# Kernel tuning notes

Measured on AMD Instinct MI355X. Metric: run time of the kernel, lower is better.

## Reference

```python
import jax, jax.numpy as jnp
import numpy as np

N_NODES = 50000
N_EDGES = 1_600_000
D = 64


def setup_inputs() -> dict:
    key = jax.random.key(0)
    k1, k2, k3, k4 = jax.random.split(key, 4)
    x = jax.random.normal(k1, (N_NODES, D), dtype=jnp.float32)
    # Glorot-ish scale for the dense transform
    weight = jax.random.normal(k2, (D, D), dtype=jnp.float32) * (1.0 / np.sqrt(D))
    bias = jnp.zeros((D,), dtype=jnp.float32)
    src = jax.random.randint(k3, (N_EDGES,), 0, N_NODES, dtype=jnp.int32)
    dst = jax.random.randint(k4, (N_EDGES,), 0, N_NODES, dtype=jnp.int32)
    t = jnp.zeros((1,), dtype=jnp.float32)
    return {"t": t, "x": x, "weight": weight, "bias": bias, "src": src, "dst": dst}


def reference(t, x, weight, bias, src, dst):
    # GCDEFunc.forward(t, x) -> GCNLayer(x); dropout=0 (eval / ODE solve).
    n = x.shape[0]
    # symmetric GCN normalization: 1/sqrt(in_degree), 0 for isolated nodes
    deg = jax.ops.segment_sum(jnp.ones_like(dst, dtype=x.dtype), dst, num_segments=n)
    norm = jnp.where(deg > 0, jax.lax.rsqrt(jnp.maximum(deg, 1.0)), 0.0)[:, None]  # [N,1]
    h = x @ weight                 # [N,D] dense transform
    h = h * norm                   # src-side normalization
    # SpMM: sum messages copy_src(h) over incoming edges
    h = jax.ops.segment_sum(h[src], dst, num_segments=n)  # [N,D]
    h = h * norm + bias            # dst-side normalization + bias
    return jax.nn.softplus(h)      # smooth activation for ODE dynamics
```

## Files before the change

### kernel.cpp

```cpp
#include <hip/hip_runtime.h>
#include <hip/hip_fp16.h>

constexpr int N = 50000;
constexpr int D = 64;
constexpr int E = 1600000;
constexpr int NBUCK = (N + 127) / 128;
constexpr int CAP = 4608;
constexpr int BTHREADS = 512;
constexpr int BBLOCKS = 512;
constexpr int EPB = E / BBLOCKS;
constexpr int CPT = (EPB + BTHREADS - 1) / BTHREADS;

__global__ void k_init(int* __restrict__ cursor) {
    int t = threadIdx.x;
    if (t < NBUCK) cursor[t] = t * CAP;
}

__global__ void k_bucket(const int* __restrict__ src, const int* __restrict__ dst,
                         int* __restrict__ cursor, unsigned* __restrict__ packed) {
    __shared__ int lh[NBUCK];
    __shared__ int scanI[NBUCK];
    __shared__ int wsum[8];
    __shared__ int lb[NBUCK];
    __shared__ unsigned stage[EPB];
    int tid = threadIdx.x;
    if (tid < NBUCK) lh[tid] = 0;
    __syncthreads();
    int base_e = blockIdx.x * EPB;
    unsigned pk[CPT];
    int bn[CPT], rk[CPT];
#pragma unroll
    for (int i = 0; i < CPT; ++i) {
        int idx = i * BTHREADS + tid;
        if (idx < EPB) {
            int e = base_e + idx;
            int d = dst[e];
            int s = src[e];
            bn[i] = d >> 7;
            pk[i] = ((unsigned)d << 16) | (unsigned)s;
            rk[i] = atomicAdd(&lh[bn[i]], 1);
        } else bn[i] = -1;
    }
    __syncthreads();
    int w = tid >> 6, l = tid & 63;
    int v = (tid < NBUCK) ? lh[tid] : 0;
    for (int off = 1; off < 64; off <<= 1) {
        int t = __shfl_up(v, off, 64);
        if (l >= off) v += t;
    }
    if (tid < NBUCK) scanI[tid] = v;
    if (l == 63) wsum[w] = v;
    __syncthreads();
    if (tid < 64) {
        int s = (tid < 8) ? wsum[tid] : 0;
        for (int off = 1; off < 8; off <<= 1) {
            int t = __shfl_up(s, off, 64);
            if (tid >= off) s += t;
        }
        if (tid < 8) wsum[tid] = s;
    }
    __syncthreads();
    if (tid < NBUCK && w > 0) scanI[tid] += wsum[w - 1];
    if (tid < NBUCK) {
        int c = lh[tid];
        lb[tid] = c ? atomicAdd(&cursor[tid], c) : 0;
    }
    __syncthreads();
#pragma unroll
    for (int i = 0; i < CPT; ++i) {
        if (bn[i] >= 0) {
            int eb = (bn[i] == 0) ? 0 : scanI[bn[i] - 1];
            stage[eb + rk[i]] = pk[i];
        }
    }
    __syncthreads();
    for (int j = tid; j < EPB; j += BTHREADS) {
        unsigned vv = stage[j];
        int bk = vv >> 23;
        int eb = (bk == 0) ? 0 : scanI[bk - 1];
        packed[lb[bk] + (j - eb)] = vv;
    }
}

__global__ void k_csr(const int* __restrict__ cursor, const unsigned* __restrict__ packed,
                      unsigned short* __restrict__ csr, int* __restrict__ rowptr,
                      int* __restrict__ rowend, float* __restrict__ norm) {
    __shared__ int cnt[128];
    __shared__ int sm[128];
    __shared__ int cur[128];
    __shared__ unsigned short stage[CAP];
    int b = blockIdx.x, tid = threadIdx.x;
    if (tid < 128) cnt[tid] = 0;
    __syncthreads();
    int beg = b * CAP;
    int m = cursor[b] - beg;
    for (int j = tid; j < m; j += 1024)
        atomicAdd(&cnt[(packed[beg + j] >> 16) & 127], 1);
    __syncthreads();
    if (tid < 64) {
        int a = cnt[2 * tid], c1 = cnt[2 * tid + 1];
        int s = a + c1;
        for (int off = 1; off < 64; off <<= 1) {
            int t = __shfl_up(s, off, 64);
            if (tid >= off) s += t;
        }
        sm[2 * tid + 1] = s;
        sm[2 * tid] = s - c1;
    }
    __syncthreads();
    if (tid < 128) {
        int incl = sm[tid];
        int excl = incl - cnt[tid];
        int node = b * 128 + tid;
        if (node < N) {
            rowptr[node] = beg + excl;
            rowend[node] = beg + incl;
            norm[node] = cnt[tid] ? rsqrtf((float)cnt[tid]) : 0.0f;
        }
        cur[tid] = excl;
    }
    __syncthreads();
    for (int j = tid; j < m; j += 1024) {
        unsigned p = packed[beg + j];
        int slot = atomicAdd(&cur[(p >> 16) & 127], 1);
        stage[slot] = (unsigned short)(p & 0xFFFFu);
    }
    __syncthreads();
    unsigned* du = (unsigned*)(csr + beg);
    const unsigned* su = (const unsigned*)stage;
    int mu = m >> 1;
    for (int k = tid; k < mu; k += 1024) du[k] = su[k];
    if ((m & 1) && tid == 0) csr[beg + m - 1] = stage[m - 1];
}

__global__ __launch_bounds__(256)
void k_gemm(const float* __restrict__ x, const float* __restrict__ W,
            const float* __restrict__ norm, __half* __restrict__ h2) {
    __shared__ float xT[64 * 68];
    __shared__ float Wl[64 * 64];
    int tid = threadIdx.x;
    int rowbase = blockIdx.x * 64;
    {
        const float4* W4 = (const float4*)W;
        float4* Wl4 = (float4*)Wl;
#pragma unroll
        for (int i = 0; i < 4; ++i)
            Wl4[i * 256 + tid] = W4[i * 256 + tid];
    }
    {
        int rr = tid >> 2;
        int c0 = (tid & 3) * 16;
        int row = rowbase + rr;
        if (row >= N) row = N - 1;
        const float4* xr = (const float4*)(x + (size_t)row * 64 + c0);
#pragma unroll
        for (int i = 0; i < 4; ++i) {
            float4 v = xr[i];
            int c = c0 + i * 4;
            xT[(c + 0) * 68 + rr] = v.x;
            xT[(c + 1) * 68 + rr] = v.y;
            xT[(c + 2) * 68 + rr] = v.z;
            xT[(c + 3) * 68 + rr] = v.w;
        }
    }
    __syncthreads();
    int tx = tid & 15;
    int ty = tid >> 4;
    float acc[4][4] = {};
#pragma unroll 8
    for (int k = 0; k < 64; ++k) {
        float4 xv = *(const float4*)&xT[k * 68 + ty * 4];
        float4 wv = *(const float4*)&Wl[k * 64 + tx * 4];
        acc[0][0] = fmaf(xv.x, wv.x, acc[0][0]);
        acc[0][1] = fmaf(xv.x, wv.y, acc[0][1]);
        acc[0][2] = fmaf(xv.x, wv.z, acc[0][2]);
        acc[0][3] = fmaf(xv.x, wv.w, acc[0][3]);
        acc[1][0] = fmaf(xv.y, wv.x, acc[1][0]);
        acc[1][1] = fmaf(xv.y, wv.y, acc[1][1]);
        acc[1][2] = fmaf(xv.y, wv.z, acc[1][2]);
        acc[1][3] = fmaf(xv.y, wv.w, acc[1][3]);
        acc[2][0] = fmaf(xv.z, wv.x, acc[2][0]);
        acc[2][1] = fmaf(xv.z, wv.y, acc[2][1]);
        acc[2][2] = fmaf(xv.z, wv.z, acc[2][2]);
        acc[2][3] = fmaf(xv.z, wv.w, acc[2][3]);
        acc[3][0] = fmaf(xv.w, wv.x, acc[3][0]);
        acc[3][1] = fmaf(xv.w, wv.y, acc[3][1]);
        acc[3][2] = fmaf(xv.w, wv.z, acc[3][2]);
        acc[3][3] = fmaf(xv.w, wv.w, acc[3][3]);
    }
#pragma unroll
    for (int i = 0; i < 4; ++i) {
        int row = rowbase + ty * 4 + i;
        if (row < N) {
            float nr = norm[row];
            __half2 p0 = __floats2half2_rn(acc[i][0] * nr, acc[i][1] * nr);
            __half2 p1 = __floats2half2_rn(acc[i][2] * nr, acc[i][3] * nr);
            __half2* dst2 = (__half2*)(h2 + (size_t)row * 64 + tx * 4);
            dst2[0] = p0;
            dst2[1] = p1;
        }
    }
}

__global__ void k_aggregate(const int* __restrict__ rowptr, const int* __restrict__ rowend,
                            const unsigned short* __restrict__ csr,
                            const __half* __restrict__ h2, const float* __restrict__ norm,
                            const float* __restrict__ bias, float* __restrict__ out) {
    int node = blockIdx.x * 4 + (threadIdx.x >> 6);
    int lane = threadIdx.x & 63;
    int half = lane >> 5;
    int fl = lane & 31;
    const __half2* h2v = (const __half2*)h2;
    int beg = rowptr[node];
    int end = rowend[node];
    int deg = end - beg;
    int myidx = (beg + lane < end) ? (int)csr[beg + lane] : 0;
    int window = deg < 64 ? deg : 64;
    int npair = window >> 1;
    float ax = 0.0f, ay = 0.0f, bx = 0.0f, by = 0.0f;
    int p = 0;
    for (; p + 7 < npair; p += 8) {
        int s0 = __shfl(myidx, 2 * p + half, 64);
        int s1 = __shfl(myidx, 2 * p + 2 + half, 64);
        int s2 = __shfl(myidx, 2 * p + 4 + half, 64);
        int s3 = __shfl(myidx, 2 * p + 6 + half, 64);
        int s4 = __shfl(myidx, 2 * p + 8 + half, 64);
        int s5 = __shfl(myidx, 2 * p + 10 + half, 64);
        int s6 = __shfl(myidx, 2 * p + 12 + half, 64);
        int s7 = __shfl(myidx, 2 * p + 14 + half, 64);
        float2 v0 = __half22float2(h2v[s0 * 32 + fl]);
        float2 v1 = __half22float2(h2v[s1 * 32 + fl]);
        float2 v2 = __half22float2(h2v[s2 * 32 + fl]);
        float2 v3 = __half22float2(h2v[s3 * 32 + fl]);
        float2 v4 = __half22float2(h2v[s4 * 32 + fl]);
        float2 v5 = __half22float2(h2v[s5 * 32 + fl]);
        float2 v6 = __half22float2(h2v[s6 * 32 + fl]);
        float2 v7 = __half22float2(h2v[s7 * 32 + fl]);
        ax += (v0.x + v2.x) + (v4.x + v6.x);
        ay += (v0.y + v2.y) + (v4.y + v6.y);
        bx += (v1.x + v3.x) + (v5.x + v7.x);
        by += (v1.y + v3.y) + (v5.y + v7.y);
    }
    for (; p + 3 < npair; p += 4) {
        int s0 = __shfl(myidx, 2 * p + half, 64);
        int s1 = __shfl(myidx, 2 * p + 2 + half, 64);
        int s2 = __shfl(myidx, 2 * p + 4 + half, 64);
        int s3 = __shfl(myidx, 2 * p + 6 + half, 64);
        float2 v0 = __half22float2(h2v[s0 * 32 + fl]);
        float2 v1 = __half22float2(h2v[s1 * 32 + fl]);
        float2 v2 = __half22float2(h2v[s2 * 32 + fl]);
        float2 v3 = __half22float2(h2v[s3 * 32 + fl]);
        ax += v0.x + v2.x;  ay += v0.y + v2.y;
        bx += v1.x + v3.x;  by += v1.y + v3.y;
    }
    for (; p < npair; ++p) {
        int s = __shfl(myidx, 2 * p + half, 64);
        float2 v = __half22float2(h2v[s * 32 + fl]);
        ax += v.x;  ay += v.y;
    }
    if (window & 1) {
        int s = __shfl(myidx, window - 1, 64);
        float2 v = __half22float2(h2v[s * 32 + fl]);
        if (half == 0) { ax += v.x;  ay += v.y; }
    }
    if (deg > 64) {
        int j = beg + 64;
        for (; j + 1 < end; j += 2) {
            int s = csr[j + half];
            float2 v = __half22float2(h2v[s * 32 + fl]);
            ax += v.x;  ay += v.y;
        }
        if (j < end) {
            int s = csr[j];
            float2 v = __half22float2(h2v[s * 32 + fl]);
            if (half == 0) { ax += v.x;  ay += v.y; }
        }
    }
    ax += bx;  ay += by;
    ax += __shfl_xor(ax, 32, 64);
    ay += __shfl_xor(ay, 32, 64);
    if (half == 0) {
        float nrm = norm[node];
        float2 bs = ((const float2*)bias)[fl];
        float vx = ax * nrm + bs.x;
        float vy = ay * nrm + bs.y;
        float2 o;
        o.x = fmaxf(vx, 0.0f) + log1pf(expf(-fabsf(vx)));
        o.y = fmaxf(vy, 0.0f) + log1pf(expf(-fabsf(vy)));
        ((float2*)out)[node * 32 + fl] = o;
    }
}

extern "C" void kernel_launch(void* const* d_in, const int* in_sizes, int n_in,
                              void* d_out, int out_size, void* d_ws, size_t ws_size,
                              hipStream_t stream) {
    const float* x    = (const float*)d_in[1];
    const float* W    = (const float*)d_in[2];
    const float* bias = (const float*)d_in[3];
    const int* src = (const int*)d_in[4];
    const int* dst = (const int*)d_in[5];
    float* out = (float*)d_out;

    char* ws = (char*)d_ws;
    __half*         h2     = (__half*)(ws);
    unsigned*       packed = (unsigned*)(ws + 6400000);
    unsigned short* csr    = (unsigned short*)(ws + 13606912);
    int*            rowptr = (int*)(ws + 17210368);
    int*            rowend = (int*)(ws + 17410368);
    float*          norm   = (float*)(ws + 17610368);
    int*            cursor = (int*)(ws + 17810368);

    k_init     <<<1, 512, 0, stream>>>(cursor);
    k_bucket   <<<BBLOCKS, BTHREADS, 0, stream>>>(src, dst, cursor, packed);
    k_csr      <<<NBUCK, 1024, 0, stream>>>(cursor, packed, csr, rowptr, rowend, norm);
    k_gemm     <<<(N + 63) / 64, 256, 0, stream>>>(x, W, norm, h2);
    k_aggregate<<<(N + 3) / 4, 256, 0, stream>>>(rowptr, rowend, csr, h2, norm, bias, out);
}
```

Baseline: 148.8 us.

## Fuse CSR build into aggregation and compute degrees with global atomics

Removes the separate CSR kernel. Each aggregation block now sorts its own 128-node bucket into a shared-memory CSR and aggregates straight from it, which drops the global csr, rowptr, rowend and norm arrays along with one kernel launch. Degrees come from global atomicAdds in the bucketing kernel so the GEMM can apply the source normalization without the CSR pass. The cost is 1.6M global atomics and only 391 large blocks of 1024 threads for the gather phase, which may lower occupancy and load balance.

Result: slower. 221.2 us (+48.7%).

```diff
diff --git a/kernel.cpp b/kernel.cpp
--- a/kernel.cpp
+++ b/kernel.cpp
@@ -11,13 +11,15 @@
 constexpr int EPB = E / BBLOCKS;
 constexpr int CPT = (EPB + BTHREADS - 1) / BTHREADS;
 
-__global__ void k_init(int* __restrict__ cursor) {
-    int t = threadIdx.x;
-    if (t < NBUCK) cursor[t] = t * CAP;
+__global__ void k_init(int* __restrict__ cursor, int* __restrict__ deg) {
+    int i = blockIdx.x * 512 + threadIdx.x;
+    if (i < N) deg[i] = 0;
+    if (i < NBUCK) cursor[i] = i * CAP;
 }
 
 __global__ void k_bucket(const int* __restrict__ src, const int* __restrict__ dst,
-                         int* __restrict__ cursor, unsigned* __restrict__ packed) {
+                         int* __restrict__ cursor, unsigned* __restrict__ packed,
+                         int* __restrict__ deg) {
     __shared__ int lh[NBUCK];
     __shared__ int scanI[NBUCK];
     __shared__ int wsum[8];
@@ -39,6 +41,7 @@
             bn[i] = d >> 7;
             pk[i] = ((unsigned)d << 16) | (unsigned)s;
             rk[i] = atomicAdd(&lh[bn[i]], 1);
+            atomicAdd(&deg[d], 1);
         } else bn[i] = -1;
     }
     __syncthreads();
@@ -82,60 +85,9 @@
     }
 }
 
-__global__ void k_csr(const int* __restrict__ cursor, const unsigned* __restrict__ packed,
-                      unsigned short* __restrict__ csr, int* __restrict__ rowptr,
-                      int* __restrict__ rowend, float* __restrict__ norm) {
-    __shared__ int cnt[128];
-    __shared__ int sm[128];
-    __shared__ int cur[128];
-    __shared__ unsigned short stage[CAP];
-    int b = blockIdx.x, tid = threadIdx.x;
-    if (tid < 128) cnt[tid] = 0;
-    __syncthreads();
-    int beg = b * CAP;
-    int m = cursor[b] - beg;
-    for (int j = tid; j < m; j += 1024)
-        atomicAdd(&cnt[(packed[beg + j] >> 16) & 127], 1);
-    __syncthreads();
-    if (tid < 64) {
-        int a = cnt[2 * tid], c1 = cnt[2 * tid + 1];
-        int s = a + c1;
-        for (int off = 1; off < 64; off <<= 1) {
-            int t = __shfl_up(s, off, 64);
-            if (tid >= off) s += t;
-        }
-        sm[2 * tid + 1] = s;
-        sm[2 * tid] = s - c1;
-    }
-    __syncthreads();
-    if (tid < 128) {
-        int incl = sm[tid];
-        int excl = incl - cnt[tid];
-        int node = b * 128 + tid;
-        if (node < N) {
-            rowptr[node] = beg + excl;
-            rowend[node] = beg + incl;
-            norm[node] = cnt[tid] ? rsqrtf((float)cnt[tid]) : 0.0f;
-        }
-        cur[tid] = excl;
-    }
-    __syncthreads();
-    for (int j = tid; j < m; j += 1024) {
-        unsigned p = packed[beg + j];
-        int slot = atomicAdd(&cur[(p >> 16) & 127], 1);
-        stage[slot] = (unsigned short)(p & 0xFFFFu);
-    }
-    __syncthreads();
-    unsigned* du = (unsigned*)(csr + beg);
-    const unsigned* su = (const unsigned*)stage;
-    int mu = m >> 1;
-    for (int k = tid; k < mu; k += 1024) du[k] = su[k];
-    if ((m & 1) && tid == 0) csr[beg + m - 1] = stage[m - 1];
-}
-
 __global__ __launch_bounds__(256)
 void k_gemm(const float* __restrict__ x, const float* __restrict__ W,
-            const float* __restrict__ norm, __half* __restrict__ h2) {
+            const int* __restrict__ deg, __half* __restrict__ h2) {
     __shared__ float xT[64 * 68];
     __shared__ float Wl[64 * 64];
     int tid = threadIdx.x;
@@ -192,7 +144,8 @@
     for (int i = 0; i < 4; ++i) {
         int row = rowbase + ty * 4 + i;
         if (row < N) {
-            float nr = norm[row];
+            int dg = deg[row];
+            float nr = dg ? rsqrtf((float)dg) : 0.0f;
             __half2 p0 = __floats2half2_rn(acc[i][0] * nr, acc[i][1] * nr);
             __half2 p1 = __floats2half2_rn(acc[i][2] * nr, acc[i][3] * nr);
             __half2* dst2 = (__half2*)(h2 + (size_t)row * 64 + tx * 4);
@@ -202,92 +155,136 @@
     }
 }
 
-__global__ void k_aggregate(const int* __restrict__ rowptr, const int* __restrict__ rowend,
-                            const unsigned short* __restrict__ csr,
-                            const __half* __restrict__ h2, const float* __restrict__ norm,
-                            const float* __restrict__ bias, float* __restrict__ out) {
-    int node = blockIdx.x * 4 + (threadIdx.x >> 6);
-    int lane = threadIdx.x & 63;
+__global__ __launch_bounds__(1024, 8)
+void k_fused(const int* __restrict__ cursor, const unsigned* __restrict__ packed,
+             const __half* __restrict__ h2, const float* __restrict__ bias,
+             float* __restrict__ out) {
+    __shared__ int cnt[128];
+    __shared__ int rowoff[128];
+    __shared__ int rowend_s[128];
+    __shared__ unsigned short stage[CAP];
+    int b = blockIdx.x, tid = threadIdx.x;
+    if (tid < 128) cnt[tid] = 0;
+    __syncthreads();
+    int beg = b * CAP;
+    int m = cursor[b] - beg;
+    unsigned pk[5];
+    int rk[5], dd[5];
+#pragma unroll
+    for (int it = 0; it < 5; ++it) {
+        int j = it * 1024 + tid;
+        if (j < m) {
+            unsigned p = packed[beg + j];
+            int d = (p >> 16) & 127;
+            dd[it] = d;
+            pk[it] = p;
+            rk[it] = atomicAdd(&cnt[d], 1);
+        } else dd[it] = -1;
+    }
+    __syncthreads();
+    if (tid < 64) {
+        int a = cnt[2 * tid], c1 = cnt[2 * tid + 1];
+        int s = a + c1;
+        for (int off = 1; off < 64; off <<= 1) {
+            int t = __shfl_up(s, off, 64);
+            if (tid >= off) s += t;
+        }
+        rowend_s[2 * tid + 1] = s;
+        rowend_s[2 * tid]     = s - c1;
+        rowoff[2 * tid + 1]   = s - c1;
+        rowoff[2 * tid]       = s - c1 - a;
+    }
+    __syncthreads();
+#pragma unroll
+    for (int it = 0; it < 5; ++it)
+        if (dd[it] >= 0)
+            stage[rowoff[dd[it]] + rk[it]] = (unsigned short)(pk[it] & 0xFFFFu);
+    __syncthreads();
+    int wv = tid >> 6, lane = tid & 63;
     int half = lane >> 5;
     int fl = lane & 31;
     const __half2* h2v = (const __half2*)h2;
-    int beg = rowptr[node];
-    int end = rowend[node];
-    int deg = end - beg;
-    int myidx = (beg + lane < end) ? (int)csr[beg + lane] : 0;
-    int window = deg < 64 ? deg : 64;
-    int npair = window >> 1;
-    float ax = 0.0f, ay = 0.0f, bx = 0.0f, by = 0.0f;
-    int p = 0;
-    for (; p + 7 < npair; p += 8) {
-        int s0 = __shfl(myidx, 2 * p + half, 64);
-        int s1 = __shfl(myidx, 2 * p + 2 + half, 64);
-        int s2 = __shfl(myidx, 2 * p + 4 + half, 64);
-        int s3 = __shfl(myidx, 2 * p + 6 + half, 64);
-        int s4 = __shfl(myidx, 2 * p + 8 + half, 64);
-        int s5 = __shfl(myidx, 2 * p + 10 + half, 64);
-        int s6 = __shfl(myidx, 2 * p + 12 + half, 64);
-        int s7 = __shfl(myidx, 2 * p + 14 + half, 64);
-        float2 v0 = __half22float2(h2v[s0 * 32 + fl]);
-        float2 v1 = __half22float2(h2v[s1 * 32 + fl]);
-        float2 v2 = __half22float2(h2v[s2 * 32 + fl]);
-        float2 v3 = __half22float2(h2v[s3 * 32 + fl]);
-        float2 v4 = __half22float2(h2v[s4 * 32 + fl]);
-        float2 v5 = __half22float2(h2v[s5 * 32 + fl]);
-        float2 v6 = __half22float2(h2v[s6 * 32 + fl]);
-        float2 v7 = __half22float2(h2v[s7 * 32 + fl]);
-        ax += (v0.x + v2.x) + (v4.x + v6.x);
-        ay += (v0.y + v2.y) + (v4.y + v6.y);
-        bx += (v1.x + v3.x) + (v5.x + v7.x);
-        by += (v1.y + v3.y) + (v5.y + v7.y);
-    }
-    for (; p + 3 < npair; p += 4) {
-        int s0 = __shfl(myidx, 2 * p + half, 64);
-        int s1 = __shfl(myidx, 2 * p + 2 + half, 64);
-        int s2 = __shfl(myidx, 2 * p + 4 + half, 64);
-        int s3 = __shfl(myidx, 2 * p + 6 + half, 64);
-        float2 v0 = __half22float2(h2v[s0 * 32 + fl]);
-        float2 v1 = __half22float2(h2v[s1 * 32 + fl]);
-        float2 v2 = __half22float2(h2v[s2 * 32 + fl]);
-        float2 v3 = __half22float2(h2v[s3 * 32 + fl]);
-        ax += v0.x + v2.x;  ay += v0.y + v2.y;
-        bx += v1.x + v3.x;  by += v1.y + v3.y;
-    }
-    for (; p < npair; ++p) {
-        int s = __shfl(myidx, 2 * p + half, 64);
-        float2 v = __half22float2(h2v[s * 32 + fl]);
-        ax += v.x;  ay += v.y;
-    }
-    if (window & 1) {
-        int s = __shfl(myidx, window - 1, 64);
-        float2 v = __half22float2(h2v[s * 32 + fl]);
-        if (half == 0) { ax += v.x;  ay += v.y; }
-    }
-    if (deg > 64) {
-        int j = beg + 64;
-        for (; j + 1 < end; j += 2) {
-            int s = csr[j + half];
+    float2 bs = ((const float2*)bias)[fl];
+    for (int i = 0; i < 8; ++i) {
+        int r = wv * 8 + i;
+        int node = b * 128 + r;
+        int rb = rowoff[r];
+        int re = rowend_s[r];
+        int deg = re - rb;
+        int myidx = (rb + lane < re) ? (int)stage[rb + lane] : 0;
+        int window = deg < 64 ? deg : 64;
+        int npair = window >> 1;
+        float ax = 0.0f, ay = 0.0f, bx = 0.0f, by = 0.0f;
+        int p = 0;
+        for (; p + 7 < npair; p += 8) {
+            int s0 = __shfl(myidx, 2 * p + half, 64);
+            int s1 = __shfl(myidx, 2 * p + 2 + half, 64);
+            int s2 = __shfl(myidx, 2 * p + 4 + half, 64);
+            int s3 = __shfl(myidx, 2 * p + 6 + half, 64);
+            int s4 = __shfl(myidx, 2 * p + 8 + half, 64);
+            int s5 = __shfl(myidx, 2 * p + 10 + half, 64);
+            int s6 = __shfl(myidx, 2 * p + 12 + half, 64);
+            int s7 = __shfl(myidx, 2 * p + 14 + half, 64);
+            float2 v0 = __half22float2(h2v[s0 * 32 + fl]);
+            float2 v1 = __half22float2(h2v[s1 * 32 + fl]);
+            float2 v2 = __half22float2(h2v[s2 * 32 + fl]);
+            float2 v3 = __half22float2(h2v[s3 * 32 + fl]);
+            float2 v4 = __half22float2(h2v[s4 * 32 + fl]);
+            float2 v5 = __half22float2(h2v[s5 * 32 + fl]);
+            float2 v6 = __half22float2(h2v[s6 * 32 + fl]);
+            float2 v7 = __half22float2(h2v[s7 * 32 + fl]);
+            ax += (v0.x + v2.x) + (v4.x + v6.x);
+            ay += (v0.y + v2.y) + (v4.y + v6.y);
+            bx += (v1.x + v3.x) + (v5.x + v7.x);
+            by += (v1.y + v3.y) + (v5.y + v7.y);
+        }
+        for (; p + 3 < npair; p += 4) {
+            int s0 = __shfl(myidx, 2 * p + half, 64);
+            int s1 = __shfl(myidx, 2 * p + 2 + half, 64);
+            int s2 = __shfl(myidx, 2 * p + 4 + half, 64);
+            int s3 = __shfl(myidx, 2 * p + 6 + half, 64);
+            float2 v0 = __half22float2(h2v[s0 * 32 + fl]);
+            float2 v1 = __half22float2(h2v[s1 * 32 + fl]);
+            float2 v2 = __half22float2(h2v[s2 * 32 + fl]);
+            float2 v3 = __half22float2(h2v[s3 * 32 + fl]);
+            ax += v0.x + v2.x;  ay += v0.y + v2.y;
+            bx += v1.x + v3.x;  by += v1.y + v3.y;
+        }
+        for (; p < npair; ++p) {
+            int s = __shfl(myidx, 2 * p + half, 64);
             float2 v = __half22float2(h2v[s * 32 + fl]);
             ax += v.x;  ay += v.y;
         }
-        if (j < end) {
-            int s = csr[j];
+        if (window & 1) {
+            int s = __shfl(myidx, window - 1, 64);
             float2 v = __half22float2(h2v[s * 32 + fl]);
             if (half == 0) { ax += v.x;  ay += v.y; }
         }
-    }
-    ax += bx;  ay += by;
-    ax += __shfl_xor(ax, 32, 64);
-    ay += __shfl_xor(ay, 32, 64);
-    if (half == 0) {
-        float nrm = norm[node];
-        float2 bs = ((const float2*)bias)[fl];
-        float vx = ax * nrm + bs.x;
-        float vy = ay * nrm + bs.y;
-        float2 o;
-        o.x = fmaxf(vx, 0.0f) + log1pf(expf(-fabsf(vx)));
-        o.y = fmaxf(vy, 0.0f) + log1pf(expf(-fabsf(vy)));
-        ((float2*)out)[node * 32 + fl] = o;
+        if (deg > 64) {
+            int j = rb + 64;
+            for (; j + 1 < re; j += 2) {
+                int s = stage[j + half];
+                float2 v = __half22float2(h2v[s * 32 + fl]);
+                ax += v.x;  ay += v.y;
+            }
+            if (j < re) {
+                int s = stage[j];
+                float2 v = __half22float2(h2v[s * 32 + fl]);
+                if (half == 0) { ax += v.x;  ay += v.y; }
+            }
+        }
+        ax += bx;  ay += by;
+        ax += __shfl_xor(ax, 32, 64);
+        ay += __shfl_xor(ay, 32, 64);
+        if (half == 0 && node < N) {
+            float nrm = deg ? rsqrtf((float)deg) : 0.0f;
+            float vx = ax * nrm + bs.x;
+            float vy = ay * nrm + bs.y;
+            float2 o;
+            o.x = fmaxf(vx, 0.0f) + log1pf(expf(-fabsf(vx)));
+            o.y = fmaxf(vy, 0.0f) + log1pf(expf(-fabsf(vy)));
+            ((float2*)out)[node * 32 + fl] = o;
+        }
     }
 }
 
@@ -302,17 +299,13 @@
     float* out = (float*)d_out;
 
     char* ws = (char*)d_ws;
-    __half*         h2     = (__half*)(ws);
-    unsigned*       packed = (unsigned*)(ws + 6400000);
-    unsigned short* csr    = (unsigned short*)(ws + 13606912);
-    int*            rowptr = (int*)(ws + 17210368);
-    int*            rowend = (int*)(ws + 17410368);
-    float*          norm   = (float*)(ws + 17610368);
-    int*            cursor = (int*)(ws + 17810368);
-
-    k_init     <<<1, 512, 0, stream>>>(cursor);
-    k_bucket   <<<BBLOCKS, BTHREADS, 0, stream>>>(src, dst, cursor, packed);
-    k_csr      <<<NBUCK, 1024, 0, stream>>>(cursor, packed, csr, rowptr, rowend, norm);
-    k_gemm     <<<(N + 63) / 64, 256, 0, stream>>>(x, W, norm, h2);
-    k_aggregate<<<(N + 3) / 4, 256, 0, stream>>>(rowptr, rowend, csr, h2, norm, bias, out);
-}
+    __half*   h2     = (__half*)(ws);
+    unsigned* packed = (unsigned*)(ws + 6400000);
+    int*      deg    = (int*)(ws + 13606912);
+    int*      cursor = (int*)(ws + 13806912);
+
+    k_init  <<<(N + 511) / 512, 512, 0, stream>>>(cursor, deg);
+    k_bucket<<<BBLOCKS, BTHREADS, 0, stream>>>(src, dst, cursor, packed, deg);
+    k_gemm  <<<(N + 63) / 64, 256, 0, stream>>>(x, W, deg, h2);
+    k_fused <<<NBUCK, 1024, 0, stream>>>(cursor, packed, h2, bias, out);
+}
```
